# Performance work log

Measured on AMD Instinct MI355X. Metric: run time of the kernel, lower is better.

## Reference

```python
import jax, jax.numpy as jnp
import numpy as np

N = 50000      # nodes
E = 800000     # edges (avg degree 16)
IN = 128       # in_channels
OUT = 2        # out_channels
HID = 100 * OUT  # MAX_CHANNELS * out_channels = 200
MSG_EPS = 1e-7   # GENConv message eps
BN_EPS = 1e-5    # BatchNorm1d eps


def _gen_conv(x, src, dst, w1, b1, g, be, w2, b2):
    """PyG GENConv with defaults: aggr='softmax', t=1.0, msg_norm=False,
    MLP=[c, 2c, c_out] with BatchNorm1d+ReLU between layers (train-mode BN)."""
    # message: relu(x_j) + eps  -> [E, d]
    msg = jnp.maximum(x[src], 0.0) + MSG_EPS
    # scatter softmax over incoming edges of each destination node (t=1)
    m = jax.ops.segment_max(msg, dst, num_segments=N)          # [N, d]
    m = jnp.where(jnp.isfinite(m), m, 0.0)                      # isolated nodes
    ex = jnp.exp(msg - m[dst])                                  # [E, d]
    s = jax.ops.segment_sum(ex, dst, num_segments=N)            # [N, d]
    alpha = ex / (s[dst] + 1e-16)                               # [E, d]
    out = jax.ops.segment_sum(msg * alpha, dst, num_segments=N) # [N, d]
    out = out + x                                               # residual with x_dst
    # MLP: Linear -> BatchNorm(batch stats) -> ReLU -> Linear
    h = out @ w1 + b1                                           # [N, 2d]
    mu = h.mean(axis=0)
    var = h.var(axis=0)
    h = (h - mu) * jax.lax.rsqrt(var + BN_EPS) * g + be
    h = jnp.maximum(h, 0.0)
    return h @ w2 + b2


def setup_inputs() -> dict:
    key = jax.random.key(0)
    ks = jax.random.split(key, 8)
    rn = lambda k, shp, s: jax.random.normal(k, shp, jnp.float32) * s
    mid1, mid2 = 2 * IN, 2 * HID
    return {
        "x": rn(ks[0], (N, IN), 1.0),
        "edge_index": jax.random.randint(ks[1], (2, E), 0, N, jnp.int32),
        "c1_w1": rn(ks[2], (IN, mid1), 0.05), "c1_b1": jnp.zeros((mid1,), jnp.float32),
        "c1_g": jnp.ones((mid1,), jnp.float32), "c1_beta": jnp.zeros((mid1,), jnp.float32),
        "c1_w2": rn(ks[3], (mid1, HID), 0.05), "c1_b2": jnp.zeros((HID,), jnp.float32),
        "c2_w1": rn(ks[4], (HID, mid2), 0.05), "c2_b1": jnp.zeros((mid2,), jnp.float32),
        "c2_g": jnp.ones((mid2,), jnp.float32), "c2_beta": jnp.zeros((mid2,), jnp.float32),
        "c2_w2": rn(ks[5], (mid2, OUT), 0.05), "c2_b2": jnp.zeros((OUT,), jnp.float32),
    }


def reference(x, edge_index, c1_w1, c1_b1, c1_g, c1_beta, c1_w2, c1_b2,
              c2_w1, c2_b1, c2_g, c2_beta, c2_w2, c2_b2):
    src, dst = edge_index[0], edge_index[1]
    h = jnp.maximum(_gen_conv(x, src, dst, c1_w1, c1_b1, c1_g, c1_beta, c1_w2, c1_b2), 0.0)
    # Dropout(p=0.1) is identity in eval mode (deterministic reference)
    return jnp.maximum(_gen_conv(h, src, dst, c2_w1, c2_b1, c2_g, c2_beta, c2_w2, c2_b2), 0.0)
```

## Files before the change

kernel.cpp:

```cpp
#include <hip/hip_runtime.h>
#include <hip/hip_bf16.h>
#include <stdint.h>

#define NNODES 50000
#define NEDGES 800000
#define DIN 128
#define DHID 200
#define MID1 256
#define MID2 400
#define NBB ((NNODES + 127) / 128)
#define RSPLIT 12
#define LOG2E 1.4426950408889634f
#define LN2 0.6931471805599453f
#define GK_SPLIT 96
#define GCH 208
#define GNP 40
#define NBUCK 98
#define BCAP 16384
#define EPB 4096

typedef __hip_bfloat16 bf16;
typedef __attribute__((ext_vector_type(8))) short short8;
typedef __attribute__((ext_vector_type(4))) float floatx4;
typedef unsigned short ushort;

__device__ __forceinline__ float b2f(bf16 v) { return __bfloat162float(v); }
__device__ __forceinline__ bf16 f2b(float v) { return __float2bfloat16(v); }
__device__ __forceinline__ float bits2f(ushort b) {
    unsigned u = ((unsigned)b) << 16;
    return __uint_as_float(u);
}
__device__ __forceinline__ ushort f2bits(float f) {
    bf16 h = __float2bfloat16(f);
    return *(ushort*)&h;
}
__device__ __forceinline__ float ldin(const void* p, size_t i, int f32) {
    return f32 ? ((const float*)p)[i] : __bfloat162float(((const bf16*)p)[i]);
}
__device__ __forceinline__ void ldin4(const void* p, size_t i, int f32, float* v) {
    if (f32) {
        float4 f = *(const float4*)((const float*)p + i);
        v[0] = f.x; v[1] = f.y; v[2] = f.z; v[3] = f.w;
    } else {
        ushort4 u = *(const ushort4*)((const bf16*)p + i);
        v[0] = bits2f(u.x); v[1] = bits2f(u.y); v[2] = bits2f(u.z); v[3] = bits2f(u.w);
    }
}
__device__ __forceinline__ float fexp2(float x) {
#if __has_builtin(__builtin_amdgcn_exp2f)
    return __builtin_amdgcn_exp2f(x);
#else
    return exp2f(x);
#endif
}
__device__ __forceinline__ floatx4 mfma16(short8 a, short8 b, floatx4 c) {
    return __builtin_amdgcn_mfma_f32_16x16x32_bf16(a, b, c, 0, 0, 0);
}
__device__ __forceinline__ void acc4(ushort4 u, float* s, float* p) {
    ushort uu[4];
    *(ushort4*)uu = u;
#pragma unroll
    for (int c = 0; c < 4; c++) {
        float v = bits2f(uu[c]);
        float ee = fexp2(v);
        s[c] += ee;
        p[c] = fmaf(v, ee, p[c]);
    }
}

__global__ __launch_bounds__(256) void bin_kernel(const int* __restrict__ src,
                                                  const int* __restrict__ dst,
                                                  const void* __restrict__ g,
                                                  int* __restrict__ flag,
                                                  unsigned* __restrict__ bbuf,
                                                  int* __restrict__ gcur) {
    __shared__ int cnt[NBUCK], cur[NBUCK];
    int tid = threadIdx.x;
    if (blockIdx.x == 0 && tid == 0)
        *flag = (((const unsigned*)g)[0] == 0x3F800000u) ? 1 : 0;
    if (tid < NBUCK) cnt[tid] = 0;
    __syncthreads();
    int e0 = blockIdx.x * EPB;
    unsigned pk[16];
    int bk[16];
#pragma unroll
    for (int i = 0; i < 16; i++) {
        int e = e0 + i * 256 + tid;
        if (e < NEDGES) {
            int d = dst[e], s = src[e];
            pk[i] = ((unsigned)d << 16) | (unsigned)s;
            bk[i] = d >> 9;
            atomicAdd(&cnt[bk[i]], 1);
        } else {
            bk[i] = -1;
        }
    }
    __syncthreads();
    if (tid < NBUCK) cur[tid] = atomicAdd(&gcur[tid], cnt[tid]);
    __syncthreads();
#pragma unroll
    for (int i = 0; i < 16; i++) {
        if (bk[i] >= 0) {
            int off = atomicAdd(&cur[bk[i]], 1);
            bbuf[(size_t)bk[i] * BCAP + off] = pk[i];
        }
    }
}

__global__ __launch_bounds__(512) void histscanA_kernel(const unsigned* __restrict__ bbuf,
                                                        const int* __restrict__ gcur,
                                                        int* __restrict__ rowptr,
                                                        int* __restrict__ blocksums) {
    __shared__ int hc[512];
    int b = blockIdx.x, t = threadIdx.x;
    int base = b << 9;
    int nn = min(512, NNODES - base);
    hc[t] = 0;
    __syncthreads();
    int cnt = gcur[b];
    const unsigned* eb = bbuf + (size_t)b * BCAP;
    for (int i = t; i < cnt; i += 512) atomicAdd(&hc[(eb[i] >> 16) - base], 1);
    __syncthreads();
    int v = hc[t];
#pragma unroll
    for (int off = 1; off < 512; off <<= 1) {
        int o = (t >= off) ? hc[t - off] : 0;
        __syncthreads();
        hc[t] += o;
        __syncthreads();
    }
    if (t < nn) rowptr[base + t] = hc[t] - v;
    if (t == 511) blocksums[b] = hc[511];
}

__global__ __launch_bounds__(512) void scanscatter_kernel(const unsigned* __restrict__ bbuf,
                                                          const int* __restrict__ gcur,
                                                          const int* __restrict__ blocksums,
                                                          int* __restrict__ rowptr,
                                                          int* __restrict__ ssrc) {
    __shared__ int sh[128];
    __shared__ int lc[512];
    int b = blockIdx.x, t = threadIdx.x;
    int base = b << 9;
    int nn = min(512, NNODES - base);
    if (t < 128) sh[t] = (t < NBUCK) ? blocksums[t] : 0;
    __syncthreads();
#pragma unroll
    for (int off = 1; off < 128; off <<= 1) {
        int o = (t < 128 && t >= off) ? sh[t - off] : 0;
        __syncthreads();
        if (t < 128) sh[t] += o;
        __syncthreads();
    }
    int boff = (b > 0) ? sh[b - 1] : 0;
    if (t < nn) {
        int r = rowptr[base + t] + boff;
        rowptr[base + t] = r;
        lc[t] = r;
    }
    if (b == NBUCK - 1 && t == 0) rowptr[NNODES] = NEDGES;
    __syncthreads();
    int cnt = gcur[b];
    const unsigned* eb = bbuf + (size_t)b * BCAP;
    for (int i = t; i < cnt; i += 512) {
        unsigned p = eb[i];
        int node = (int)(p >> 16) - base;
        int idx = atomicAdd(&lc[node], 1);
        ssrc[idx] = (int)(p & 0xFFFFu);
    }
}

#define TW (DIN * MID1 + MID1 * DHID + DHID * MID2)
__global__ __launch_bounds__(256) void prep_kernel(const void* __restrict__ W1, bf16* __restrict__ Wt1,
                                                   const void* __restrict__ W2, bf16* __restrict__ Wt2,
                                                   const void* __restrict__ W3, bf16* __restrict__ Wt3,
                                                   const void* __restrict__ X, bf16* __restrict__ M1,
                                                   ushort* __restrict__ dummy,
                                                   const int* __restrict__ flag) {
    const int S1 = DIN * MID1, S2 = MID1 * DHID;
    int f32 = *flag;
    int idx = blockIdx.x * 256 + threadIdx.x;
    if (idx < TW) {
        const void* W;
        bf16* Wt;
        int K, N, li;
        if (idx < S1) { W = W1; Wt = Wt1; K = DIN; N = MID1; li = idx; }
        else if (idx < S1 + S2) { W = W2; Wt = Wt2; K = MID1; N = DHID; li = idx - S1; }
        else { W = W3; Wt = Wt3; K = DHID; N = MID2; li = idx - S1 - S2; }
        int k = li / N, n = li - k * N;
        Wt[(size_t)n * K + k] = f2b(ldin(W, li, f32));
    }
    if (idx < DHID) dummy[idx] = 0xC300;
    int i = idx * 4;
    if (i < NNODES * DIN) {
        float v[4];
        ldin4(X, i, f32, v);
        ushort4 o;
        o.x = f2bits((fmaxf(v[0], 0.f) + 1e-7f) * LOG2E);
        o.y = f2bits((fmaxf(v[1], 0.f) + 1e-7f) * LOG2E);
        o.z = f2bits((fmaxf(v[2], 0.f) + 1e-7f) * LOG2E);
        o.w = f2bits((fmaxf(v[3], 0.f) + 1e-7f) * LOG2E);
        *(ushort4*)(M1 + i) = o;
    }
}

__global__ __launch_bounds__(256) void agg1_kernel(const void* __restrict__ X,
                                                   const bf16* __restrict__ M1,
                                                   const int* __restrict__ rowptr,
                                                   const int* __restrict__ ssrc,
                                                   const int* __restrict__ flag,
                                                   bf16* __restrict__ out) {
    int f32 = *flag;
    int hl = threadIdx.x & 31;
    int n = blockIdx.x * 8 + (threadIdx.x >> 5);
    int r0 = rowptr[n];
    int deg = rowptr[n + 1] - r0;
    const char* M1b = (const char*)M1;
    int boff = hl << 3;
    float s[4] = {0.f, 0.f, 0.f, 0.f}, p[4] = {0.f, 0.f, 0.f, 0.f};
    for (int base = 0; base < deg; base += 32) {
        int cnt = min(32, deg - base);
        int eo = ((base + hl < deg) ? ssrc[r0 + base + hl] : 0) << 8;
        int i = 0;
        for (; i + 7 < cnt; i += 8) {
            ushort4 u[8];
#pragma unroll
            for (int k = 0; k < 8; k++) {
                int o = __shfl(eo, i + k, 32) + boff;
                u[k] = *(const ushort4*)(M1b + o);
            }
#pragma unroll
            for (int k = 0; k < 8; k++) acc4(u[k], s, p);
        }
        for (; i < cnt; i++) {
            int o = __shfl(eo, i, 32) + boff;
            acc4(*(const ushort4*)(M1b + o), s, p);
        }
    }
    float xc[4];
    ldin4(X, (size_t)n * DIN + 4 * hl, f32, xc);
    ushort4 o;
    o.x = f2bits(fmaf(LN2, p[0] / (s[0] + 1e-16f), xc[0]));
    o.y = f2bits(fmaf(LN2, p[1] / (s[1] + 1e-16f), xc[1]));
    o.z = f2bits(fmaf(LN2, p[2] / (s[2] + 1e-16f), xc[2]));
    o.w = f2bits(fmaf(LN2, p[3] / (s[3] + 1e-16f), xc[3]));
    *(ushort4*)(out + (size_t)n * DIN + 4 * hl) = o;
}

__global__ __launch_bounds__(256) void agg2_kernel(const bf16* __restrict__ M2,
                                                   const int* __restrict__ rowptr,
                                                   const int* __restrict__ ssrc,
                                                   const ushort* __restrict__ dummy,
                                                   bf16* __restrict__ out) {
    int lane = threadIdx.x & 63;
    int n = blockIdx.x * 4 + (threadIdx.x >> 6);
    int r0 = __builtin_amdgcn_readfirstlane(rowptr[n]);
    int deg = __builtin_amdgcn_readfirstlane(rowptr[n + 1]) - r0;
    bool act = lane < 50;
    int boff = (act ? lane : 49) << 3;
    const char* M2b = (const char*)M2;
    const char* dp = (const char*)dummy;
    float s[4] = {0.f, 0.f, 0.f, 0.f}, p[4] = {0.f, 0.f, 0.f, 0.f};
    int nfull = deg >> 3;
    for (int b = 0; b < nfull; b++) {
        const int* ep = ssrc + r0 + (b << 3);
        ushort4 u[8];
#pragma unroll
        for (int k = 0; k < 8; k++)
            u[k] = *(const ushort4*)(M2b + (size_t)((unsigned)ep[k] * 400u) + boff);
#pragma unroll
        for (int k = 0; k < 8; k++) acc4(u[k], s, p);
    }
    int rem = deg & 7;
    if (rem) {
        const int* ep = ssrc + r0 + (nfull << 3);
        ushort4 u[8];
#pragma unroll
        for (int k = 0; k < 8; k++) {
            const char* rp = (k < rem) ? (M2b + (size_t)((unsigned)ep[k] * 400u)) : dp;
            u[k] = *(const ushort4*)(rp + boff);
        }
#pragma unroll
        for (int k = 0; k < 8; k++) acc4(u[k], s, p);
    }
    if (act) {
        ushort4 u = *(const ushort4*)(M2b + (size_t)n * 400 + boff);
        float vn[4] = {bits2f(u.x), bits2f(u.y), bits2f(u.z), bits2f(u.w)};
        ushort4 o;
        o.x = f2bits(LN2 * (p[0] / (s[0] + 1e-16f) + vn[0]) - 1e-7f);
        o.y = f2bits(LN2 * (p[1] / (s[1] + 1e-16f) + vn[1]) - 1e-7f);
        o.z = f2bits(LN2 * (p[2] / (s[2] + 1e-16f) + vn[2]) - 1e-7f);
        o.w = f2bits(LN2 * (p[3] / (s[3] + 1e-16f) + vn[3]) - 1e-7f);
        *(ushort4*)(out + (size_t)n * DHID + 4 * lane) = o;
    }
}

template <int MODE, int NT, int KK, int NCOL>
__global__ __launch_bounds__(512, 4) void bgemm(const bf16* __restrict__ A,
                                                const bf16* __restrict__ Bt,
                                                const void* __restrict__ bias,
                                                const int* __restrict__ flag,
                                                const float* __restrict__ sc,
                                                const float* __restrict__ offs,
                                                const float* __restrict__ bnsum,
                                                const float* __restrict__ bnsumsq,
                                                const void* __restrict__ gam,
                                                const void* __restrict__ bet,
                                                const void* __restrict__ w2,
                                                bf16* __restrict__ Out, int ostride,
                                                float* __restrict__ psum,
                                                float* __restrict__ psq,
                                                float* __restrict__ fscr, int M) {
    constexpr int KP = (KK + 31) & ~31;
    constexpr int KS = KP / 32;
    constexpr int KV8 = KP / 8;
    __shared__ short Bs[NT * 16][KP + 8];
    __shared__ float scs[MODE == 1 ? KK : 1];
    __shared__ float ofs[MODE == 1 ? KK : 1];
    int f32 = *flag;
    int tid = threadIdx.x;
    int cb = blockIdx.y * NCOL;

    if (MODE == 1) {
        for (int c = tid; c < KK; c += 512) {
            float mu = bnsum[c] / (float)NNODES;
            float var = fmaxf(bnsumsq[c] / (float)NNODES - mu * mu, 0.f);
            float rstd = rsqrtf(var + 1e-5f);
            float sv = rstd * ldin(gam, c, f32);
            scs[c] = sv;
            ofs[c] = ldin(bet, c, f32) - mu * sv;
        }
    }
    for (int idx = tid; idx < NT * 16 * KV8; idx += 512) {
        int col = idx / KV8, kq = (idx - col * KV8) * 8;
        uint4 v = {0, 0, 0, 0};
        if (col < NCOL && kq < KK) v = *(const uint4*)(Bt + (size_t)(cb + col) * KK + kq);
        *(uint4*)&Bs[col][kq] = v;
    }
    __syncthreads();

    int w = tid >> 6, L = tid & 63;
    int lm = L & 15, q = L >> 4;
    int rw = blockIdx.x * 128 + w * 16;
    int ar = rw + lm;
    bool rok = ar < M;

    uint4 af[KS];
#pragma unroll
    for (int s = 0; s < KS; s++) {
        int k = s * 32 + q * 8;
        af[s] = (uint4){0, 0, 0, 0};
        if (rok && k + 8 <= KK) af[s] = *(const uint4*)(A + (size_t)ar * KK + k);
    }

    floatx4 acc[NT];
#pragma unroll
    for (int t = 0; t < NT; t++) acc[t] = (floatx4){0.f, 0.f, 0.f, 0.f};

#pragma unroll
    for (int s = 0; s < KS; s++) {
        short8 as;
        if (MODE == 1) {
            int ch = s * 32 + q * 8;
            ushort us[8];
            *(uint4*)us = af[s];
#pragma unroll
            for (int j = 0; j < 8; j++)
                us[j] = f2bits(fmaxf(fmaf(bits2f(us[j]), scs[ch + j], ofs[ch + j]), 0.f));
            as = *(short8*)us;
        } else {
            as = *(short8*)&af[s];
        }
#pragma unroll
        for (int t = 0; t < NT; t++) {
            short8 bf = *(const short8*)&Bs[t * 16 + lm][s * 32 + q * 8];
            acc[t] = mfma16(as, bf, acc[t]);
        }
    }

    if (MODE == 0) {
#pragma unroll
        for (int t = 0; t < NT; t++) {
            int col = t * 16 + lm;
            float bb = ldin(bias, col, f32);
            float cs = 0.f, cq = 0.f;
#pragma unroll
            for (int r = 0; r < 4; r++) {
                int gm = rw + q * 4 + r;
                if (gm < M) {
                    float v = acc[t][r] + bb;
                    Out[(size_t)gm * ostride + col] = f2b(v);
                    cs += v;
                    cq += v * v;
                }
            }
            cs += __shfl_xor(cs, 16, 64); cq += __shfl_xor(cq, 16, 64);
            cs += __shfl_xor(cs, 32, 64); cq += __shfl_xor(cq, 32, 64);
            if (q == 0) {
                psum[(size_t)(blockIdx.x * 8 + w) * (NT * 16) + col] = cs;
                psq[(size_t)(blockIdx.x * 8 + w) * (NT * 16) + col] = cq;
            }
        }
    }
    if (MODE == 1) {
#pragma unroll
        for (int t = 0; t < NT; t++) {
            int col = t * 16 + lm;
            if (col < NCOL) {
                int gg = cb + col;
                float bb = ldin(bias, gg, f32);
#pragma unroll
                for (int r = 0; r < 4; r++) {
                    int gm = rw + q * 4 + r;
                    if (gm < M) {
                        float v = acc[t][r] + bb;
                        Out[(size_t)gm * ostride + gg] = f2b((fmaxf(v, 0.f) + 1e-7f) * LOG2E);
                    }
                }
            }
        }
    }
    if (MODE == 2) {
        float s0[4] = {0.f, 0.f, 0.f, 0.f}, s1[4] = {0.f, 0.f, 0.f, 0.f};
#pragma unroll
        for (int t = 0; t < NT; t++) {
            int col = t * 16 + lm;
            if (col < NCOL) {
                int gg = cb + col;
                float bb = ldin(bias, gg, f32);
                float scv = sc[gg], ofv = offs[gg];
                float w20 = ldin(w2, 2 * gg, f32), w21 = ldin(w2, 2 * gg + 1, f32);
#pragma unroll
                for (int r = 0; r < 4; r++) {
                    float vn = fmaxf((acc[t][r] + bb) * scv + ofv, 0.f);
                    s0[r] = fmaf(vn, w20, s0[r]);
                    s1[r] = fmaf(vn, w21, s1[r]);
                }
            }
        }
#pragma unroll
        for (int d = 1; d < 16; d <<= 1) {
#pragma unroll
            for (int r = 0; r < 4; r++) {
                s0[r] += __shfl_xor(s0[r], d, 64);
                s1[r] += __shfl_xor(s1[r], d, 64);
            }
        }
        if (lm == 0) {
#pragma unroll
            for (int r = 0; r < 4; r++) {
                int gm = rw + q * 4 + r;
                if (gm < M) {
                    fscr[(size_t)gm * 8 + blockIdx.y * 2 + 0] = s0[r];
                    fscr[(size_t)gm * 8 + blockIdx.y * 2 + 1] = s1[r];
                }
            }
        }
    }
}

__global__ __launch_bounds__(256) void stats_reduce(const float* __restrict__ psum,
                                                    const float* __restrict__ psq,
                                                    float* __restrict__ bnsum,
                                                    float* __restrict__ bnsumsq,
                                                    int NB, int NC) {
    __shared__ float shs[4][64], shq[4][64];
    int cc = threadIdx.x & 63;
    int c = blockIdx.x * 64 + cc;
    int ro = threadIdx.x >> 6;
    int chunk = (NB + RSPLIT - 1) / RSPLIT;
    int b0 = blockIdx.y * chunk;
    int b1 = min(b0 + chunk, NB);
    float s = 0.f, sq = 0.f;
    if (c < NC) {
        for (int b = b0 + ro; b < b1; b += 4) {
            s += psum[(size_t)b * NC + c];
            sq += psq[(size_t)b * NC + c];
        }
    }
    shs[ro][cc] = s;
    shq[ro][cc] = sq;
    __syncthreads();
    if (threadIdx.x < 64) {
        int gc = blockIdx.x * 64 + threadIdx.x;
        if (gc < NC) {
            int t = threadIdx.x;
            float ts = shs[0][t] + shs[1][t] + shs[2][t] + shs[3][t];
            float tq = shq[0][t] + shq[1][t] + shq[2][t] + shq[3][t];
            atomicAdd(&bnsum[gc], ts);
            atomicAdd(&bnsumsq[gc], tq);
        }
    }
}

__global__ __launch_bounds__(512) void gram_kernel(const bf16* __restrict__ X,
                                                   float* __restrict__ pg) {
    __shared__ short T[GCH][GNP];
    int tid = threadIdx.x;
    int w = tid >> 6, L = tid & 63;
    int lm = L & 15, q = L >> 4;
    floatx4 acc[2][13];
#pragma unroll
    for (int c = 0; c < 2; c++)
#pragma unroll
        for (int t = 0; t < 13; t++) acc[c][t] = (floatx4){0.f, 0.f, 0.f, 0.f};

    const int chunks = (NNODES + 32 * GK_SPLIT - 1) / (32 * GK_SPLIT);
    int base0 = blockIdx.x * chunks * 32;
    for (int ch = 0; ch < chunks; ch++) {
        int nb = base0 + ch * 32;
#pragma unroll
        for (int p = 0; p < 4; p++) {
            int idx = tid + p * 512;
            if (idx < 1600) {
                int nl = idx & 31, cq = idx >> 5;
                int gn = nb + nl;
                ushort4 u = {0, 0, 0, 0};
                if (gn < NNODES) u = *(const ushort4*)(X + (size_t)gn * DHID + cq * 4);
                T[cq * 4 + 0][nl] = (short)u.x;
                T[cq * 4 + 1][nl] = (short)u.y;
                T[cq * 4 + 2][nl] = (short)u.z;
                T[cq * 4 + 3][nl] = (short)u.w;
            }
        }
        if (tid < 256) {
            int nl = tid & 31, c = 200 + (tid >> 5);
            int gn = nb + nl;
            T[c][nl] = (c == 200 && gn < NNODES) ? (short)0x3F80 : (short)0;
        }
        __syncthreads();
        short8 af[13];
#pragma unroll
        for (int t = 0; t < 13; t++) af[t] = *(const short8*)&T[t * 16 + lm][q * 8];
#pragma unroll
        for (int c = 0; c < 2; c++) {
            int cj = w + c * 8;
            if (cj < 13) {
                short8 bf = *(const short8*)&T[cj * 16 + lm][q * 8];
#pragma unroll
                for (int t = 0; t < 13; t++) acc[c][t] = mfma16(af[t], bf, acc[c][t]);
            }
        }
        __syncthreads();
    }
    float* pgb = pg + (size_t)blockIdx.x * (GCH * GCH);
#pragma unroll
    for (int c = 0; c < 2; c++) {
        int cj = w + c * 8;
        if (cj < 13) {
#pragma unroll
            for (int t = 0; t < 13; t++)
#pragma unroll
                for (int r = 0; r < 4; r++)
                    pgb[(size_t)(t * 16 + q * 4 + r) * GCH + cj * 16 + lm] = acc[c][t][r];
        }
    }
}

__global__ void greduce_kernel(const float* __restrict__ pg, float* __restrict__ G) {
    int e = blockIdx.x * 256 + threadIdx.x;
    if (e < GCH * GCH) {
        float s = 0.f;
        for (int b = 0; b < GK_SPLIT; b++) s += pg[(size_t)b * (GCH * GCH) + e];
        G[e] = s;
    }
}

__global__ __launch_bounds__(256) void bn2_finish(const float* __restrict__ G,
                                                  const bf16* __restrict__ Wt3,
                                                  const void* __restrict__ b1,
                                                  const void* __restrict__ g,
                                                  const void* __restrict__ be,
                                                  const int* __restrict__ flag,
                                                  float* __restrict__ sc,
                                                  float* __restrict__ off) {
    __shared__ float wl[200];
    __shared__ float red[256];
    __shared__ float dsh;
    int f32 = *flag;
    int c = blockIdx.x;
    int t = threadIdx.x;
    if (t < 200) wl[t] = b2f(Wt3[(size_t)c * DHID + t]);
    __syncthreads();
    float di = 0.f;
    if (t <= 200) {
        const float* Gr = G + (size_t)t * GCH;
        for (int j = 0; j < 200; j++) di = fmaf(Gr[j], wl[j], di);
    }
    red[t] = (t < 200) ? wl[t] * di : 0.f;
    if (t == 200) dsh = di;
    __syncthreads();
    for (int o = 128; o > 0; o >>= 1) {
        if (t < o) red[t] += red[t + o];
        __syncthreads();
    }
    if (t == 0) {
        float d = dsh;
        float bc = ldin(b1, c, f32);
        float mu = d / (float)NNODES + bc;
        float eh2 = (red[0] + 2.f * bc * d) / (float)NNODES + bc * bc;
        float var = fmaxf(eh2 - mu * mu, 0.f);
        float rstd = rsqrtf(var + 1e-5f);
        float s = rstd * ldin(g, c, f32);
        sc[c] = s;
        off[c] = ldin(be, c, f32) - mu * s;
    }
}

__global__ void final_combine(const float* __restrict__ fscr, const void* __restrict__ b2,
                              const int* __restrict__ flag, void* __restrict__ outp, int M) {
    int f32 = *flag;
    int n = blockIdx.x * 256 + threadIdx.x;
    if (n < M) {
        const float* f = fscr + (size_t)n * 8;
        float v0 = fmaxf(f[0] + f[2] + f[4] + f[6] + ldin(b2, 0, f32), 0.f);
        float v1 = fmaxf(f[1] + f[3] + f[5] + f[7] + ldin(b2, 1, f32), 0.f);
        if (f32) {
            ((float*)outp)[2 * n] = v0;
            ((float*)outp)[2 * n + 1] = v1;
        } else {
            ((bf16*)outp)[2 * n] = f2b(v0);
            ((bf16*)outp)[2 * n + 1] = f2b(v1);
        }
    }
}

extern "C" void kernel_launch(void* const* d_in, const int* in_sizes, int n_in,
                              void* d_out, int out_size, void* d_ws, size_t ws_size,
                              hipStream_t stream) {
    const void* x = d_in[0];
    const int* ei = (const int*)d_in[1];
    const void* c1_w1 = d_in[2];
    const void* c1_b1 = d_in[3];
    const void* c1_g = d_in[4];
    const void* c1_be = d_in[5];
    const void* c1_w2 = d_in[6];
    const void* c1_b2 = d_in[7];
    const void* c2_w1 = d_in[8];
    const void* c2_b1 = d_in[9];
    const void* c2_g = d_in[10];
    const void* c2_be = d_in[11];
    const void* c2_w2 = d_in[12];
    const void* c2_b2 = d_in[13];

    const int* src = ei;
    const int* dst = ei + NEDGES;

    uint8_t* w = (uint8_t*)d_ws;
    int* rowptr = (int*)(w + 0);
    bf16* wT1 = (bf16*)(w + 204800);
    bf16* wT2 = (bf16*)(w + 270336);
    bf16* wT3 = (bf16*)(w + 409600);
    int* ssrc = (int*)(w + 614400);
    float* bnbuf = (float*)(w + 3814400);
    float* sum1 = bnbuf, *sumsq1 = bnbuf + 256;
    int* gcur = (int*)(bnbuf + 512);
    float* sc2 = bnbuf + 1824, *off2 = bnbuf + 2224;
    int* flag_in = (int*)(bnbuf + 2624);
    int* blocksums = (int*)(bnbuf + 2640);
    ushort* dummyrow = (ushort*)(bnbuf + 2840);
    uint8_t* bufA = w + 3830784;
    uint8_t* bufB = w + 23830784;
    unsigned* bbuf = (unsigned*)bufA;
    bf16* out1 = (bf16*)bufA;
    bf16* h1 = (bf16*)bufA;
    float* fscr = (float*)bufA;
    float* pg = (float*)bufA;
    float* Gm = (float*)(bufA + 17000000);
    bf16* M1 = (bf16*)bufB;
    bf16* t1 = (bf16*)bufB;
    bf16* out2 = (bf16*)bufB;
    float* ps1 = (float*)(bufA + 12800000);
    float* pq1 = ps1 + (size_t)NBB * 8 * MID1;

    hipMemsetAsync(bnbuf, 0, 1312 * sizeof(float), stream);

    bin_kernel<<<(NEDGES + EPB - 1) / EPB, 256, 0, stream>>>(src, dst, c1_g, flag_in,
                                                             bbuf, gcur);
    histscanA_kernel<<<NBUCK, 512, 0, stream>>>(bbuf, gcur, rowptr, blocksums);
    scanscatter_kernel<<<NBUCK, 512, 0, stream>>>(bbuf, gcur, blocksums, rowptr, ssrc);

    prep_kernel<<<(NNODES * DIN / 4 + 255) / 256, 256, 0, stream>>>(
        c1_w1, wT1, c1_w2, wT2, c2_w1, wT3, x, M1, dummyrow, flag_in);

    agg1_kernel<<<NNODES / 8, 256, 0, stream>>>(x, M1, rowptr, ssrc, flag_in, out1);
    bgemm<0, 16, 128, 256><<<dim3(NBB, 1), 512, 0, stream>>>(
        out1, wT1, c1_b1, flag_in, nullptr, nullptr,
        nullptr, nullptr, nullptr, nullptr, nullptr,
        t1, MID1, ps1, pq1, nullptr, NNODES);
    stats_reduce<<<dim3((MID1 + 63) / 64, RSPLIT), 256, 0, stream>>>(ps1, pq1, sum1, sumsq1,
                                                                     NBB * 8, MID1);
    bgemm<1, 7, 256, 100><<<dim3(NBB, 2), 512, 0, stream>>>(
        t1, wT2, c1_b2, flag_in, nullptr, nullptr,
        sum1, sumsq1, c1_g, c1_be, nullptr,
        h1, DHID, nullptr, nullptr, nullptr, NNODES);

    agg2_kernel<<<NNODES / 4, 256, 0, stream>>>(h1, rowptr, ssrc, dummyrow, out2);
    gram_kernel<<<GK_SPLIT, 512, 0, stream>>>(out2, pg);
    greduce_kernel<<<(GCH * GCH + 255) / 256, 256, 0, stream>>>(pg, Gm);
    bn2_finish<<<MID2, 256, 0, stream>>>(Gm, wT3, c2_b1, c2_g, c2_be, flag_in, sc2, off2);
    bgemm<2, 7, 200, 100><<<dim3(NBB, 4), 512, 0, stream>>>(
        out2, wT3, c2_b1, flag_in, sc2, off2,
        nullptr, nullptr, nullptr, nullptr, c2_w2,
        nullptr, 0, nullptr, nullptr, fscr, NNODES);
    final_combine<<<(NNODES + 255) / 256, 256, 0, stream>>>(fscr, c2_b2, flag_in,
                                                            d_out, NNODES);
}
```

Baseline: 366.4 us.

## Fuse bin and prep kernels, fold BN stats into GEMM, widen agg1 lanes

The edge-binning and weight/feature prep kernels now run as one launch that partitions its blocks by role. Prep computes the fp32 flag locally instead of reading it from the bin kernel, which removes that dependency. The first GEMM reduces its BN column sums in shared memory and atomically adds them to global totals, so the partial-sum buffers and the stats_reduce launch are no longer needed. agg1 now gives each node a full 64-lane wave with 2 channels per lane, reads edge indices directly with a padded remainder, and the gram split count changes. The changes cut launch count and intermediate traffic, at the cost of more global float atomics and a different gather pattern.

```diff
diff --git a/kernel.cpp b/kernel.cpp
--- a/kernel.cpp
+++ b/kernel.cpp
@@ -9,15 +9,16 @@
 #define MID1 256
 #define MID2 400
 #define NBB ((NNODES + 127) / 128)
-#define RSPLIT 12
 #define LOG2E 1.4426950408889634f
 #define LN2 0.6931471805599453f
-#define GK_SPLIT 96
+#define GK_SPLIT 112
 #define GCH 208
 #define GNP 40
 #define NBUCK 98
 #define BCAP 16384
 #define EPB 4096
+#define BIN_NB ((NEDGES + EPB - 1) / EPB)
+#define PREP_NB ((NNODES * DIN / 4 + 255) / 256)
 
 typedef __hip_bfloat16 bf16;
 typedef __attribute__((ext_vector_type(8))) short short8;
@@ -67,42 +68,85 @@
         p[c] = fmaf(v, ee, p[c]);
     }
 }
-
-__global__ __launch_bounds__(256) void bin_kernel(const int* __restrict__ src,
-                                                  const int* __restrict__ dst,
-                                                  const void* __restrict__ g,
-                                                  int* __restrict__ flag,
-                                                  unsigned* __restrict__ bbuf,
-                                                  int* __restrict__ gcur) {
+__device__ __forceinline__ void acc2(ushort2 u, float* s, float* p) {
+    float v0 = bits2f(u.x), v1 = bits2f(u.y);
+    float e0 = fexp2(v0), e1 = fexp2(v1);
+    s[0] += e0;
+    p[0] = fmaf(v0, e0, p[0]);
+    s[1] += e1;
+    p[1] = fmaf(v1, e1, p[1]);
+}
+
+#define TW (DIN * MID1 + MID1 * DHID + DHID * MID2)
+__global__ __launch_bounds__(256) void binprep_kernel(const int* __restrict__ src,
+                                                      const int* __restrict__ dst,
+                                                      const void* __restrict__ g,
+                                                      int* __restrict__ flag,
+                                                      unsigned* __restrict__ bbuf,
+                                                      int* __restrict__ gcur,
+                                                      const void* __restrict__ W1, bf16* __restrict__ Wt1,
+                                                      const void* __restrict__ W2, bf16* __restrict__ Wt2,
+                                                      const void* __restrict__ W3, bf16* __restrict__ Wt3,
+                                                      const void* __restrict__ X, bf16* __restrict__ M1,
+                                                      ushort* __restrict__ dummy) {
     __shared__ int cnt[NBUCK], cur[NBUCK];
     int tid = threadIdx.x;
-    if (blockIdx.x == 0 && tid == 0)
-        *flag = (((const unsigned*)g)[0] == 0x3F800000u) ? 1 : 0;
-    if (tid < NBUCK) cnt[tid] = 0;
-    __syncthreads();
-    int e0 = blockIdx.x * EPB;
-    unsigned pk[16];
-    int bk[16];
-#pragma unroll
-    for (int i = 0; i < 16; i++) {
-        int e = e0 + i * 256 + tid;
-        if (e < NEDGES) {
-            int d = dst[e], s = src[e];
-            pk[i] = ((unsigned)d << 16) | (unsigned)s;
-            bk[i] = d >> 9;
-            atomicAdd(&cnt[bk[i]], 1);
-        } else {
-            bk[i] = -1;
-        }
-    }
-    __syncthreads();
-    if (tid < NBUCK) cur[tid] = atomicAdd(&gcur[tid], cnt[tid]);
-    __syncthreads();
-#pragma unroll
-    for (int i = 0; i < 16; i++) {
-        if (bk[i] >= 0) {
-            int off = atomicAdd(&cur[bk[i]], 1);
-            bbuf[(size_t)bk[i] * BCAP + off] = pk[i];
+    int bx = blockIdx.x;
+    if (bx < BIN_NB) {
+        if (bx == 0 && tid == 0)
+            *flag = (((const unsigned*)g)[0] == 0x3F800000u) ? 1 : 0;
+        if (tid < NBUCK) cnt[tid] = 0;
+        __syncthreads();
+        int e0 = bx * EPB;
+        unsigned pk[16];
+        int bk[16];
+#pragma unroll
+        for (int i = 0; i < 16; i++) {
+            int e = e0 + i * 256 + tid;
+            if (e < NEDGES) {
+                int d = dst[e], s = src[e];
+                pk[i] = ((unsigned)d << 16) | (unsigned)s;
+                bk[i] = d >> 9;
+                atomicAdd(&cnt[bk[i]], 1);
+            } else {
+                bk[i] = -1;
+            }
+        }
+        __syncthreads();
+        if (tid < NBUCK) cur[tid] = atomicAdd(&gcur[tid], cnt[tid]);
+        __syncthreads();
+#pragma unroll
+        for (int i = 0; i < 16; i++) {
+            if (bk[i] >= 0) {
+                int off = atomicAdd(&cur[bk[i]], 1);
+                bbuf[(size_t)bk[i] * BCAP + off] = pk[i];
+            }
+        }
+    } else {
+        int f32 = (((const unsigned*)g)[0] == 0x3F800000u) ? 1 : 0;
+        int idx = (bx - BIN_NB) * 256 + tid;
+        const int S1 = DIN * MID1, S2 = MID1 * DHID;
+        if (idx < TW) {
+            const void* W;
+            bf16* Wt;
+            int K, N, li;
+            if (idx < S1) { W = W1; Wt = Wt1; K = DIN; N = MID1; li = idx; }
+            else if (idx < S1 + S2) { W = W2; Wt = Wt2; K = MID1; N = DHID; li = idx - S1; }
+            else { W = W3; Wt = Wt3; K = DHID; N = MID2; li = idx - S1 - S2; }
+            int k = li / N, n = li - k * N;
+            Wt[(size_t)n * K + k] = f2b(ldin(W, li, f32));
+        }
+        if (idx < DHID) dummy[idx] = 0xC300;
+        int i = idx * 4;
+        if (i < NNODES * DIN) {
+            float v[4];
+            ldin4(X, i, f32, v);
+            ushort4 o;
+            o.x = f2bits((fmaxf(v[0], 0.f) + 1e-7f) * LOG2E);
+            o.y = f2bits((fmaxf(v[1], 0.f) + 1e-7f) * LOG2E);
+            o.z = f2bits((fmaxf(v[2], 0.f) + 1e-7f) * LOG2E);
+            o.w = f2bits((fmaxf(v[3], 0.f) + 1e-7f) * LOG2E);
+            *(ushort4*)(M1 + i) = o;
         }
     }
 }
@@ -170,81 +214,51 @@
     }
 }
 
-#define TW (DIN * MID1 + MID1 * DHID + DHID * MID2)
-__global__ __launch_bounds__(256) void prep_kernel(const void* __restrict__ W1, bf16* __restrict__ Wt1,
-                                                   const void* __restrict__ W2, bf16* __restrict__ Wt2,
-                                                   const void* __restrict__ W3, bf16* __restrict__ Wt3,
-                                                   const void* __restrict__ X, bf16* __restrict__ M1,
-                                                   ushort* __restrict__ dummy,
-                                                   const int* __restrict__ flag) {
-    const int S1 = DIN * MID1, S2 = MID1 * DHID;
-    int f32 = *flag;
-    int idx = blockIdx.x * 256 + threadIdx.x;
-    if (idx < TW) {
-        const void* W;
-        bf16* Wt;
-        int K, N, li;
-        if (idx < S1) { W = W1; Wt = Wt1; K = DIN; N = MID1; li = idx; }
-        else if (idx < S1 + S2) { W = W2; Wt = Wt2; K = MID1; N = DHID; li = idx - S1; }
-        else { W = W3; Wt = Wt3; K = DHID; N = MID2; li = idx - S1 - S2; }
-        int k = li / N, n = li - k * N;
-        Wt[(size_t)n * K + k] = f2b(ldin(W, li, f32));
-    }
-    if (idx < DHID) dummy[idx] = 0xC300;
-    int i = idx * 4;
-    if (i < NNODES * DIN) {
-        float v[4];
-        ldin4(X, i, f32, v);
-        ushort4 o;
-        o.x = f2bits((fmaxf(v[0], 0.f) + 1e-7f) * LOG2E);
-        o.y = f2bits((fmaxf(v[1], 0.f) + 1e-7f) * LOG2E);
-        o.z = f2bits((fmaxf(v[2], 0.f) + 1e-7f) * LOG2E);
-        o.w = f2bits((fmaxf(v[3], 0.f) + 1e-7f) * LOG2E);
-        *(ushort4*)(M1 + i) = o;
-    }
-}
-
 __global__ __launch_bounds__(256) void agg1_kernel(const void* __restrict__ X,
                                                    const bf16* __restrict__ M1,
                                                    const int* __restrict__ rowptr,
                                                    const int* __restrict__ ssrc,
+                                                   const ushort* __restrict__ dummy,
                                                    const int* __restrict__ flag,
                                                    bf16* __restrict__ out) {
     int f32 = *flag;
-    int hl = threadIdx.x & 31;
-    int n = blockIdx.x * 8 + (threadIdx.x >> 5);
-    int r0 = rowptr[n];
-    int deg = rowptr[n + 1] - r0;
+    int lane = threadIdx.x & 63;
+    int n = blockIdx.x * 4 + (threadIdx.x >> 6);
+    int r0 = __builtin_amdgcn_readfirstlane(rowptr[n]);
+    int deg = __builtin_amdgcn_readfirstlane(rowptr[n + 1]) - r0;
+    int boff = lane << 2;
     const char* M1b = (const char*)M1;
-    int boff = hl << 3;
-    float s[4] = {0.f, 0.f, 0.f, 0.f}, p[4] = {0.f, 0.f, 0.f, 0.f};
-    for (int base = 0; base < deg; base += 32) {
-        int cnt = min(32, deg - base);
-        int eo = ((base + hl < deg) ? ssrc[r0 + base + hl] : 0) << 8;
-        int i = 0;
-        for (; i + 7 < cnt; i += 8) {
-            ushort4 u[8];
-#pragma unroll
-            for (int k = 0; k < 8; k++) {
-                int o = __shfl(eo, i + k, 32) + boff;
-                u[k] = *(const ushort4*)(M1b + o);
-            }
-#pragma unroll
-            for (int k = 0; k < 8; k++) acc4(u[k], s, p);
-        }
-        for (; i < cnt; i++) {
-            int o = __shfl(eo, i, 32) + boff;
-            acc4(*(const ushort4*)(M1b + o), s, p);
-        }
-    }
-    float xc[4];
-    ldin4(X, (size_t)n * DIN + 4 * hl, f32, xc);
-    ushort4 o;
-    o.x = f2bits(fmaf(LN2, p[0] / (s[0] + 1e-16f), xc[0]));
-    o.y = f2bits(fmaf(LN2, p[1] / (s[1] + 1e-16f), xc[1]));
-    o.z = f2bits(fmaf(LN2, p[2] / (s[2] + 1e-16f), xc[2]));
-    o.w = f2bits(fmaf(LN2, p[3] / (s[3] + 1e-16f), xc[3]));
-    *(ushort4*)(out + (size_t)n * DIN + 4 * hl) = o;
+    const char* dp = (const char*)dummy;
+    float s[2] = {0.f, 0.f}, p[2] = {0.f, 0.f};
+    int nfull = deg >> 3;
+    for (int b = 0; b < nfull; b++) {
+        const int* ep = ssrc + r0 + (b << 3);
+        ushort2 u[8];
+#pragma unroll
+        for (int k = 0; k < 8; k++)
+            u[k] = *(const ushort2*)(M1b + ((size_t)(unsigned)ep[k] << 8) + boff);
+#pragma unroll
+        for (int k = 0; k < 8; k++) acc2(u[k], s, p);
+    }
+    int rem = deg & 7;
+    if (rem) {
+        const int* ep = ssrc + r0 + (nfull << 3);
+        ushort2 u[8];
+#pragma unroll
+        for (int k = 0; k < 8; k++) {
+            const char* rp = (k < rem) ? (M1b + ((size_t)(unsigned)ep[k] << 8)) : dp;
+            u[k] = *(const ushort2*)(rp + boff);
+        }
+#pragma unroll
+        for (int k = 0; k < 8; k++) acc2(u[k], s, p);
+    }
+    int c0 = lane * 2;
+    float xc0 = ldin(X, (size_t)n * DIN + c0, f32);
+    float xc1 = ldin(X, (size_t)n * DIN + c0 + 1, f32);
+    ushort2 o;
+    o.x = f2bits(fmaf(LN2, p[0] / (s[0] + 1e-16f), xc0));
+    o.y = f2bits(fmaf(LN2, p[1] / (s[1] + 1e-16f), xc1));
+    *(ushort2*)(out + (size_t)n * DIN + c0) = o;
 }
 
 __global__ __launch_bounds__(256) void agg2_kernel(const bf16* __restrict__ M2,
@@ -302,14 +316,12 @@
                                                 const int* __restrict__ flag,
                                                 const float* __restrict__ sc,
                                                 const float* __restrict__ offs,
-                                                const float* __restrict__ bnsum,
-                                                const float* __restrict__ bnsumsq,
+                                                float* __restrict__ bnsum,
+                                                float* __restrict__ bnsumsq,
                                                 const void* __restrict__ gam,
                                                 const void* __restrict__ bet,
                                                 const void* __restrict__ w2,
                                                 bf16* __restrict__ Out, int ostride,
-                                                float* __restrict__ psum,
-                                                float* __restrict__ psq,
                                                 float* __restrict__ fscr, int M) {
     constexpr int KP = (KK + 31) & ~31;
     constexpr int KS = KP / 32;
@@ -379,6 +391,9 @@
     }
 
     if (MODE == 0) {
+        float* fs = (float*)&Bs[0][0];
+        float* fq = fs + 8 * 256;
+        __syncthreads();
 #pragma unroll
         for (int t = 0; t < NT; t++) {
             int col = t * 16 + lm;
@@ -397,9 +412,20 @@
             cs += __shfl_xor(cs, 16, 64); cq += __shfl_xor(cq, 16, 64);
             cs += __shfl_xor(cs, 32, 64); cq += __shfl_xor(cq, 32, 64);
             if (q == 0) {
-                psum[(size_t)(blockIdx.x * 8 + w) * (NT * 16) + col] = cs;
-                psq[(size_t)(blockIdx.x * 8 + w) * (NT * 16) + col] = cq;
-            }
+                fs[w * 256 + col] = cs;
+                fq[w * 256 + col] = cq;
+            }
+        }
+        __syncthreads();
+        for (int c = tid; c < NT * 16; c += 512) {
+            float ts = 0.f, tq = 0.f;
+#pragma unroll
+            for (int ww = 0; ww < 8; ww++) {
+                ts += fs[ww * 256 + c];
+                tq += fq[ww * 256 + c];
+            }
+            atomicAdd(&bnsum[c], ts);
+            atomicAdd(&bnsumsq[c], tq);
         }
     }
     if (MODE == 1) {
@@ -455,40 +481,6 @@
                     fscr[(size_t)gm * 8 + blockIdx.y * 2 + 1] = s1[r];
                 }
             }
-        }
-    }
-}
-
-__global__ __launch_bounds__(256) void stats_reduce(const float* __restrict__ psum,
-                                                    const float* __restrict__ psq,
-                                                    float* __restrict__ bnsum,
-                                                    float* __restrict__ bnsumsq,
-                                                    int NB, int NC) {
-    __shared__ float shs[4][64], shq[4][64];
-    int cc = threadIdx.x & 63;
-    int c = blockIdx.x * 64 + cc;
-    int ro = threadIdx.x >> 6;
-    int chunk = (NB + RSPLIT - 1) / RSPLIT;
-    int b0 = blockIdx.y * chunk;
-    int b1 = min(b0 + chunk, NB);
-    float s = 0.f, sq = 0.f;
-    if (c < NC) {
-        for (int b = b0 + ro; b < b1; b += 4) {
-            s += psum[(size_t)b * NC + c];
-            sq += psq[(size_t)b * NC + c];
-        }
-    }
-    shs[ro][cc] = s;
-    shq[ro][cc] = sq;
-    __syncthreads();
-    if (threadIdx.x < 64) {
-        int gc = blockIdx.x * 64 + threadIdx.x;
-        if (gc < NC) {
-            int t = threadIdx.x;
-            float ts = shs[0][t] + shs[1][t] + shs[2][t] + shs[3][t];
-            float tq = shq[0][t] + shq[1][t] + shq[2][t] + shq[3][t];
-            atomicAdd(&bnsum[gc], ts);
-            atomicAdd(&bnsumsq[gc], tq);
         }
     }
 }
@@ -664,36 +656,31 @@
     unsigned* bbuf = (unsigned*)bufA;
     bf16* out1 = (bf16*)bufA;
     bf16* h1 = (bf16*)bufA;
+    float* pg = (float*)bufA;
+    float* Gm = (float*)(bufA + 19400000);
     float* fscr = (float*)bufA;
-    float* pg = (float*)bufA;
-    float* Gm = (float*)(bufA + 17000000);
     bf16* M1 = (bf16*)bufB;
     bf16* t1 = (bf16*)bufB;
     bf16* out2 = (bf16*)bufB;
-    float* ps1 = (float*)(bufA + 12800000);
-    float* pq1 = ps1 + (size_t)NBB * 8 * MID1;
 
     hipMemsetAsync(bnbuf, 0, 1312 * sizeof(float), stream);
 
-    bin_kernel<<<(NEDGES + EPB - 1) / EPB, 256, 0, stream>>>(src, dst, c1_g, flag_in,
-                                                             bbuf, gcur);
+    binprep_kernel<<<BIN_NB + PREP_NB, 256, 0, stream>>>(
+        src, dst, c1_g, flag_in, bbuf, gcur,
+        c1_w1, wT1, c1_w2, wT2, c2_w1, wT3, x, M1, dummyrow);
     histscanA_kernel<<<NBUCK, 512, 0, stream>>>(bbuf, gcur, rowptr, blocksums);
     scanscatter_kernel<<<NBUCK, 512, 0, stream>>>(bbuf, gcur, blocksums, rowptr, ssrc);
 
-    prep_kernel<<<(NNODES * DIN / 4 + 255) / 256, 256, 0, stream>>>(
-        c1_w1, wT1, c1_w2, wT2, c2_w1, wT3, x, M1, dummyrow, flag_in);
-
-    agg1_kernel<<<NNODES / 8, 256, 0, stream>>>(x, M1, rowptr, ssrc, flag_in, out1);
+    agg1_kernel<<<NNODES / 4, 256, 0, stream>>>(x, M1, rowptr, ssrc, dummyrow, flag_in,
+                                                out1);
     bgemm<0, 16, 128, 256><<<dim3(NBB, 1), 512, 0, stream>>>(
         out1, wT1, c1_b1, flag_in, nullptr, nullptr,
-        nullptr, nullptr, nullptr, nullptr, nullptr,
-        t1, MID1, ps1, pq1, nullptr, NNODES);
-    stats_reduce<<<dim3((MID1 + 63) / 64, RSPLIT), 256, 0, stream>>>(ps1, pq1, sum1, sumsq1,
-                                                                     NBB * 8, MID1);
+        sum1, sumsq1, nullptr, nullptr, nullptr,
+        t1, MID1, nullptr, NNODES);
     bgemm<1, 7, 256, 100><<<dim3(NBB, 2), 512, 0, stream>>>(
         t1, wT2, c1_b2, flag_in, nullptr, nullptr,
         sum1, sumsq1, c1_g, c1_be, nullptr,
-        h1, DHID, nullptr, nullptr, nullptr, NNODES);
+        h1, DHID, nullptr, NNODES);
 
     agg2_kernel<<<NNODES / 4, 256, 0, stream>>>(h1, rowptr, ssrc, dummyrow, out2);
     gram_kernel<<<GK_SPLIT, 512, 0, stream>>>(out2, pg);
@@ -702,7 +689,7 @@
     bgemm<2, 7, 200, 100><<<dim3(NBB, 4), 512, 0, stream>>>(
         out2, wT3, c2_b1, flag_in, sc2, off2,
         nullptr, nullptr, nullptr, nullptr, c2_w2,
-        nullptr, 0, nullptr, nullptr, fscr, NNODES);
+        nullptr, 0, fscr, NNODES);
     final_combine<<<(NNODES + 255) / 256, 256, 0, stream>>>(fscr, c2_b2, flag_in,
                                                             d_out, NNODES);
 }
```

Measured after the change: 337.2 us. 1.09x faster.
